# Kernel tuning notes

Hardware: AMD Instinct MI355X
Metric: run time of the kernel (lower is better)

## Reference

```python
import jax, jax.numpy as jnp
import numpy as np

B, N, D, D_MODEL = 4, 2048, 512, 512


def setup_inputs() -> dict:
    key = jax.random.key(0)
    kx, kq, kk, kv, ks = jax.random.split(key, 5)
    scale = 1.0 / np.sqrt(D)
    x = jax.random.normal(kx, (B, N, D), dtype=jnp.float32)
    Wq = (jax.random.normal(kq, (D, D_MODEL), dtype=jnp.float32) * scale)
    Wk = (jax.random.normal(kk, (D, D_MODEL), dtype=jnp.float32) * scale)
    Wv = (jax.random.normal(kv, (D, D_MODEL), dtype=jnp.float32) * scale)
    Ws = (jax.random.normal(ks, (D, 1), dtype=jnp.float32) * scale)
    return {"x": x, "Wq": Wq, "Wk": Wk, "Wv": Wv, "Ws": Ws}


def reference(x, Wq, Wk, Wv, Ws):
    # Projections (Linear, no bias)
    Q = x @ Wq                      # (B, N, d_model)
    K = x @ Wk                      # (B, N, d_model)
    V = x @ Wv                      # (B, N, d_model)
    sigma = x @ Ws                  # (B, N, 1)

    n = x.shape[1]
    dm = Wq.shape[1]

    # Prior association: Gaussian kernel over |i-j| distance, row-normalized
    idx = jnp.arange(n)
    dist = jnp.abs(idx[:, None] - idx[None, :]).astype(x.dtype)      # (N, N)
    inv_norm = 1.0 / (jnp.sqrt(2.0 * jnp.pi).astype(x.dtype) * jnp.abs(sigma))
    gaussian = inv_norm * jnp.exp(-0.5 * jnp.square(dist[None] / sigma))  # (B,N,N)
    P = gaussian / jnp.sum(gaussian, axis=-1, keepdims=True)

    # Series association: scaled dot-product softmax attention
    scores = jnp.einsum('bnd,bmd->bnm', Q, K) / jnp.sqrt(jnp.asarray(dm, x.dtype))
    S = jax.nn.softmax(scores, axis=-1)                               # (B,N,N)

    # Reconstruction
    Z = S @ V                                                          # (B,N,d_model)
    return (Z, P)
```

## Files before the change

kernel.cpp:

```cpp
#include <hip/hip_runtime.h>

typedef float f32x4 __attribute__((ext_vector_type(4)));
typedef short s16x8 __attribute__((ext_vector_type(8)));
typedef unsigned short us4 __attribute__((ext_vector_type(4)));

#define MFMA16(a, b, c) __builtin_amdgcn_mfma_f32_16x16x32_bf16(a, b, c, 0, 0, 0)

#define GLOAD_LDS16(gp, lp) __builtin_amdgcn_global_load_lds( \
    (__attribute__((address_space(1))) void*)(gp),            \
    (__attribute__((address_space(3))) void*)(lp), 16, 0, 0)

__device__ __forceinline__ unsigned short f2bf(float f) {
    union { float f; unsigned u; } v; v.f = f;
    unsigned r = v.u + 0x7fffu + ((v.u >> 16) & 1u);
    return (unsigned short)(r >> 16);
}

__device__ __forceinline__ void gemm_core(
    const unsigned short* __restrict__ Ab, size_t Astride,
    const unsigned short* __restrict__ Bb, size_t Bstride,
    int K, unsigned short* As, unsigned short* Bs,
    int t, f32x4 acc[4][4])
{
    const int wave = t >> 6, lane = t & 63;
    const int c = lane & 15, quad = lane >> 4;
    const int wm = (wave >> 1) * 64, wn = (wave & 1) * 64;
    const int srow = t >> 2;
    const int scol = (t & 3) * 8;

    for (int k0 = 0; k0 < K; k0 += 32) {
        __syncthreads();
        const unsigned short* ga = Ab + (size_t)srow * Astride + k0 + scol;
        const unsigned short* gb = Bb + (size_t)srow * Bstride + k0 + scol;
        GLOAD_LDS16(ga,                 As + t * 8);
        GLOAD_LDS16(ga + 64 * Astride,  As + 2048 + t * 8);
        GLOAD_LDS16(gb,                 Bs + t * 8);
        GLOAD_LDS16(gb + 64 * Bstride,  Bs + 2048 + t * 8);
        __syncthreads();

        s16x8 af[4], bf[4];
        #pragma unroll
        for (int i = 0; i < 4; i++)
            af[i] = *(const s16x8*)(As + (wm + i * 16 + c) * 32 + quad * 8);
        #pragma unroll
        for (int i = 0; i < 4; i++)
            bf[i] = *(const s16x8*)(Bs + (wn + i * 16 + c) * 32 + quad * 8);
        #pragma unroll
        for (int mt = 0; mt < 4; mt++)
            #pragma unroll
            for (int nt = 0; nt < 4; nt++)
                acc[mt][nt] = MFMA16(af[mt], bf[nt], acc[mt][nt]);
    }
}

__global__ __launch_bounds__(256) void k_convert(
    const float* __restrict__ x, const float* __restrict__ wq,
    const float* __restrict__ wk, const float* __restrict__ wv,
    unsigned short* __restrict__ xbf, unsigned short* __restrict__ wt,
    float* __restrict__ lg)
{
    int bid = blockIdx.x, t = threadIdx.x;
    if (bid < 4096) {
        int gid = bid * 256 + t;
        float4 v = ((const float4*)x)[gid];
        us4 o = { f2bf(v.x), f2bf(v.y), f2bf(v.z), f2bf(v.w) };
        ((us4*)xbf)[gid] = o;
    } else if (bid < 7168) {
        int idx = (bid - 4096) * 256 + t;
        int w = idx >> 18;
        int r = idx & 262143;
        int k = r >> 9, n = r & 511;
        const float* src = (w == 0) ? wq : (w == 1) ? wk : wv;
        wt[((size_t)(w * 512 + n) << 9) + k] = f2bf(src[r]);
    } else {
        lg[(bid - 7168) * 256 + t] = 0.f;
    }
}

__global__ __launch_bounds__(256) void k_proj(
    const unsigned short* __restrict__ xbf, const unsigned short* __restrict__ wt,
    unsigned short* __restrict__ qbf, unsigned short* __restrict__ kbf,
    unsigned short* __restrict__ vtbf)
{
    __shared__ __align__(16) unsigned short As[128 * 32];
    __shared__ __align__(16) unsigned short Bs[128 * 32];

    int t = threadIdx.x;
    int m0 = blockIdx.x * 128, n0 = blockIdx.y * 128;
    f32x4 acc[4][4] = {};

    gemm_core(xbf + (size_t)m0 * 512, 512, wt + (size_t)n0 * 512, 512,
              512, As, Bs, t, acc);

    int wave = t >> 6, lane = t & 63, c = lane & 15, quad = lane >> 4;
    int wm = (wave >> 1) * 64, wn = (wave & 1) * 64;
    int sel = blockIdx.y >> 2;

    if (sel < 2) {
        unsigned short* dst = sel ? kbf : qbf;
        int ncol0 = n0 - sel * 512;
        #pragma unroll
        for (int mt = 0; mt < 4; mt++) {
            #pragma unroll
            for (int nt = 0; nt < 4; nt++) {
                int col = ncol0 + wn + nt * 16 + c;
                #pragma unroll
                for (int r = 0; r < 4; r++) {
                    int rw = m0 + wm + mt * 16 + quad * 4 + r;
                    dst[(size_t)rw * 512 + col] = f2bf(acc[mt][nt][r]);
                }
            }
        }
    } else {
        #pragma unroll
        for (int mt = 0; mt < 4; mt++) {
            int rw0 = m0 + wm + mt * 16 + quad * 4;
            int bb = rw0 >> 11, nn = rw0 & 2047;
            #pragma unroll
            for (int nt = 0; nt < 4; nt++) {
                int d = (n0 - 1024) + wn + nt * 16 + c;
                us4 pk = { f2bf(acc[mt][nt][0]), f2bf(acc[mt][nt][1]),
                           f2bf(acc[mt][nt][2]), f2bf(acc[mt][nt][3]) };
                *(us4*)(vtbf + ((size_t)(bb * 512 + d)) * 2048 + nn) = pk;
            }
        }
    }
}

__global__ __launch_bounds__(256) void k_score(
    const unsigned short* __restrict__ qbf, const unsigned short* __restrict__ kbf,
    unsigned short* __restrict__ pbf, float* __restrict__ lg)
{
    __shared__ __align__(16) unsigned short As[128 * 32];
    __shared__ __align__(16) unsigned short Bs[128 * 32];

    int t = threadIdx.x;
    int b = blockIdx.z;
    int m0 = blockIdx.x * 128, n0 = blockIdx.y * 128;
    f32x4 acc[4][4] = {};

    gemm_core(qbf + (size_t)(b * 2048 + m0) * 512, 512,
              kbf + (size_t)(b * 2048 + n0) * 512, 512,
              512, As, Bs, t, acc);

    int wave = t >> 6, lane = t & 63, c = lane & 15, quad = lane >> 4;
    int wm = (wave >> 1) * 64, wn = (wave & 1) * 64;
    const float scale = 0.044194173824159216f;

    #pragma unroll
    for (int mt = 0; mt < 4; mt++) {
        #pragma unroll
        for (int r = 0; r < 4; r++) {
            int row = m0 + wm + mt * 16 + quad * 4 + r;
            float rs = 0.f;
            #pragma unroll
            for (int nt = 0; nt < 4; nt++) {
                float p = __expf(acc[mt][nt][r] * scale);
                rs += p;
                pbf[(size_t)(b * 2048 + row) * 2048 + n0 + wn + nt * 16 + c] = f2bf(p);
            }
            rs += __shfl_xor(rs, 1, 16);
            rs += __shfl_xor(rs, 2, 16);
            rs += __shfl_xor(rs, 4, 16);
            rs += __shfl_xor(rs, 8, 16);
            if (c == 0) atomicAdd(&lg[b * 2048 + row], rs);
        }
    }
}

__global__ __launch_bounds__(256) void k_out(
    const unsigned short* __restrict__ pbf, const unsigned short* __restrict__ vtbf,
    const float* __restrict__ lg, float* __restrict__ zout)
{
    __shared__ __align__(16) unsigned short As[128 * 32];
    __shared__ __align__(16) unsigned short Bs[128 * 32];
    __shared__ float invl[128];

    int t = threadIdx.x;
    int b = blockIdx.z;
    int m0 = blockIdx.x * 128, n0 = blockIdx.y * 128;

    if (t < 128) invl[t] = 1.0f / lg[b * 2048 + m0 + t];

    f32x4 acc[4][4] = {};
    gemm_core(pbf + (size_t)(b * 2048 + m0) * 2048, 2048,
              vtbf + (size_t)(b * 512 + n0) * 2048, 2048,
              2048, As, Bs, t, acc);

    int wave = t >> 6, lane = t & 63, c = lane & 15, quad = lane >> 4;
    int wm = (wave >> 1) * 64, wn = (wave & 1) * 64;

    #pragma unroll
    for (int mt = 0; mt < 4; mt++) {
        #pragma unroll
        for (int nt = 0; nt < 4; nt++) {
            #pragma unroll
            for (int r = 0; r < 4; r++) {
                int row = wm + mt * 16 + quad * 4 + r;
                zout[(size_t)(b * 2048 + m0 + row) * 512 + n0 + wn + nt * 16 + c]
                    = acc[mt][nt][r] * invl[row];
            }
        }
    }
}

__global__ __launch_bounds__(256) void k_prior(
    const float* __restrict__ x, const float* __restrict__ wsv,
    float* __restrict__ pout)
{
    __shared__ float red[4];
    __shared__ float red2[4];

    int blk = blockIdx.x;
    int i = blk & 2047;
    int t = threadIdx.x;
    const float* xr = x + (size_t)blk * 512;

    float part = xr[t] * wsv[t] + xr[t + 256] * wsv[t + 256];
    #pragma unroll
    for (int o = 32; o; o >>= 1) part += __shfl_xor(part, o, 64);
    if ((t & 63) == 0) red[t >> 6] = part;
    __syncthreads();
    float sigma = red[0] + red[1] + red[2] + red[3];

    float inv2 = 0.5f / (sigma * sigma);
    float g[8];
    float sum = 0.f;
    #pragma unroll
    for (int u = 0; u < 8; u++) {
        int j = t + u * 256;
        float d = (float)(j - i);
        g[u] = (j == i) ? 1.0f : __expf(-(d * d) * inv2);
        sum += g[u];
    }
    #pragma unroll
    for (int o = 32; o; o >>= 1) sum += __shfl_xor(sum, o, 64);
    if ((t & 63) == 0) red2[t >> 6] = sum;
    __syncthreads();
    float inv = 1.0f / (red2[0] + red2[1] + red2[2] + red2[3]);

    float* pr = pout + (size_t)blk * 2048;
    #pragma unroll
    for (int u = 0; u < 8; u++) pr[t + u * 256] = g[u] * inv;
}

extern "C" void kernel_launch(void* const* d_in, const int* in_sizes, int n_in,
                              void* d_out, int out_size, void* d_ws, size_t ws_size,
                              hipStream_t stream)
{
    const float* x  = (const float*)d_in[0];
    const float* wq = (const float*)d_in[1];
    const float* wk = (const float*)d_in[2];
    const float* wv = (const float*)d_in[3];
    const float* ws = (const float*)d_in[4];

    float* zout = (float*)d_out;
    float* pout = zout + (size_t)4 * 2048 * 512;

    unsigned short* base = (unsigned short*)pout;
    unsigned short* pbf  = base;
    unsigned short* qbf  = base + (size_t)16777216;
    unsigned short* kbf  = qbf  + (size_t)4194304;
    unsigned short* vtbf = kbf  + (size_t)4194304;
    float*          lg   = (float*)(vtbf + (size_t)4194304);
    unsigned short* xbf  = base;
    unsigned short* wt   = base + (size_t)4194304;

    k_convert<<<dim3(7200), dim3(256), 0, stream>>>(x, wq, wk, wv, xbf, wt, lg);
    k_proj  <<<dim3(64, 12),    dim3(256), 0, stream>>>(xbf, wt, qbf, kbf, vtbf);
    k_score <<<dim3(16, 16, 4), dim3(256), 0, stream>>>(qbf, kbf, pbf, lg);
    k_out   <<<dim3(16, 4, 4),  dim3(256), 0, stream>>>(pbf, vtbf, lg, zout);
    k_prior <<<dim3(8192),      dim3(256), 0, stream>>>(x, ws, pout);
}
```

Measured before the change: 213.6 us.

## Use workspace buffers, fuse prior into score kernel, shrink out-GEMM tile

When the workspace is large enough, the intermediates go into it instead of the P output region. That lets the prior computation run in the same launch as the score GEMM, as extra blocks, rather than in a trailing kernel. The output GEMM now uses 128x64 tiles, doubling the block count from 256 to 512 to raise occupancy. The prior kernel writes contiguous float4 stores per thread. The cost is a larger mixed kernel with uneven block work and more B-tile reloads of P in the out GEMM.

```diff
diff --git a/kernel.cpp b/kernel.cpp
--- a/kernel.cpp
+++ b/kernel.cpp
@@ -16,7 +16,7 @@
     return (unsigned short)(r >> 16);
 }
 
-__device__ __forceinline__ void gemm_core(
+__device__ __forceinline__ void gemm_core128(
     const unsigned short* __restrict__ Ab, size_t Astride,
     const unsigned short* __restrict__ Bb, size_t Bstride,
     int K, unsigned short* As, unsigned short* Bs,
@@ -89,8 +89,8 @@
     int m0 = blockIdx.x * 128, n0 = blockIdx.y * 128;
     f32x4 acc[4][4] = {};
 
-    gemm_core(xbf + (size_t)m0 * 512, 512, wt + (size_t)n0 * 512, 512,
-              512, As, Bs, t, acc);
+    gemm_core128(xbf + (size_t)m0 * 512, 512, wt + (size_t)n0 * 512, 512,
+                 512, As, Bs, t, acc);
 
     int wave = t >> 6, lane = t & 63, c = lane & 15, quad = lane >> 4;
     int wm = (wave >> 1) * 64, wn = (wave & 1) * 64;
@@ -127,21 +127,15 @@
     }
 }
 
-__global__ __launch_bounds__(256) void k_score(
+__device__ __forceinline__ void score_body(
     const unsigned short* __restrict__ qbf, const unsigned short* __restrict__ kbf,
-    unsigned short* __restrict__ pbf, float* __restrict__ lg)
-{
-    __shared__ __align__(16) unsigned short As[128 * 32];
-    __shared__ __align__(16) unsigned short Bs[128 * 32];
-
-    int t = threadIdx.x;
-    int b = blockIdx.z;
-    int m0 = blockIdx.x * 128, n0 = blockIdx.y * 128;
+    unsigned short* __restrict__ pbf, float* __restrict__ lg,
+    int b, int m0, int n0, int t, unsigned short* As, unsigned short* Bs)
+{
     f32x4 acc[4][4] = {};
-
-    gemm_core(qbf + (size_t)(b * 2048 + m0) * 512, 512,
-              kbf + (size_t)(b * 2048 + n0) * 512, 512,
-              512, As, Bs, t, acc);
+    gemm_core128(qbf + (size_t)(b * 2048 + m0) * 512, 512,
+                 kbf + (size_t)(b * 2048 + n0) * 512, 512,
+                 512, As, Bs, t, acc);
 
     int wave = t >> 6, lane = t & 63, c = lane & 15, quad = lane >> 4;
     int wm = (wave >> 1) * 64, wn = (wave & 1) * 64;
@@ -168,32 +162,125 @@
     }
 }
 
+__device__ __forceinline__ void prior_body(
+    const float* __restrict__ x, const float* __restrict__ wsv,
+    float* __restrict__ pout, int blk, int t, float* red, float* red2)
+{
+    int i = blk & 2047;
+    const float* xr = x + (size_t)blk * 512;
+
+    float part = xr[t] * wsv[t] + xr[t + 256] * wsv[t + 256];
+    #pragma unroll
+    for (int o = 32; o; o >>= 1) part += __shfl_xor(part, o, 64);
+    if ((t & 63) == 0) red[t >> 6] = part;
+    __syncthreads();
+    float sigma = red[0] + red[1] + red[2] + red[3];
+
+    float inv2 = 0.5f / (sigma * sigma);
+    float g[8];
+    float sum = 0.f;
+    int j0 = t * 8;
+    #pragma unroll
+    for (int u = 0; u < 8; u++) {
+        int j = j0 + u;
+        float d = (float)(j - i);
+        g[u] = (j == i) ? 1.0f : __expf(-(d * d) * inv2);
+        sum += g[u];
+    }
+    #pragma unroll
+    for (int o = 32; o; o >>= 1) sum += __shfl_xor(sum, o, 64);
+    if ((t & 63) == 0) red2[t >> 6] = sum;
+    __syncthreads();
+    float inv = 1.0f / (red2[0] + red2[1] + red2[2] + red2[3]);
+
+    float* pr = pout + (size_t)blk * 2048 + j0;
+    float4 o0 = { g[0] * inv, g[1] * inv, g[2] * inv, g[3] * inv };
+    float4 o1 = { g[4] * inv, g[5] * inv, g[6] * inv, g[7] * inv };
+    ((float4*)pr)[0] = o0;
+    ((float4*)pr)[1] = o1;
+}
+
+__global__ __launch_bounds__(256) void k_score_prior(
+    const unsigned short* __restrict__ qbf, const unsigned short* __restrict__ kbf,
+    unsigned short* __restrict__ pbf, float* __restrict__ lg,
+    const float* __restrict__ x, const float* __restrict__ wsv,
+    float* __restrict__ pout)
+{
+    __shared__ __align__(16) unsigned short As[128 * 32];
+    __shared__ __align__(16) unsigned short Bs[128 * 32];
+    __shared__ float red[4];
+    __shared__ float red2[4];
+
+    int bid = blockIdx.x, t = threadIdx.x;
+    if (bid < 1024) {
+        int b = bid >> 8, r = bid & 255;
+        score_body(qbf, kbf, pbf, lg, b, (r & 15) * 128, (r >> 4) * 128, t, As, Bs);
+    } else {
+        prior_body(x, wsv, pout, bid - 1024, t, red, red2);
+    }
+}
+
+__global__ __launch_bounds__(256) void k_score(
+    const unsigned short* __restrict__ qbf, const unsigned short* __restrict__ kbf,
+    unsigned short* __restrict__ pbf, float* __restrict__ lg)
+{
+    __shared__ __align__(16) unsigned short As[128 * 32];
+    __shared__ __align__(16) unsigned short Bs[128 * 32];
+    score_body(qbf, kbf, pbf, lg, blockIdx.z,
+               blockIdx.x * 128, blockIdx.y * 128, threadIdx.x, As, Bs);
+}
+
 __global__ __launch_bounds__(256) void k_out(
     const unsigned short* __restrict__ pbf, const unsigned short* __restrict__ vtbf,
     const float* __restrict__ lg, float* __restrict__ zout)
 {
     __shared__ __align__(16) unsigned short As[128 * 32];
-    __shared__ __align__(16) unsigned short Bs[128 * 32];
+    __shared__ __align__(16) unsigned short Bs[64 * 32];
     __shared__ float invl[128];
 
     int t = threadIdx.x;
     int b = blockIdx.z;
-    int m0 = blockIdx.x * 128, n0 = blockIdx.y * 128;
+    int m0 = blockIdx.x * 128, n0 = blockIdx.y * 64;
 
     if (t < 128) invl[t] = 1.0f / lg[b * 2048 + m0 + t];
 
-    f32x4 acc[4][4] = {};
-    gemm_core(pbf + (size_t)(b * 2048 + m0) * 2048, 2048,
-              vtbf + (size_t)(b * 512 + n0) * 2048, 2048,
-              2048, As, Bs, t, acc);
-
-    int wave = t >> 6, lane = t & 63, c = lane & 15, quad = lane >> 4;
-    int wm = (wave >> 1) * 64, wn = (wave & 1) * 64;
+    const unsigned short* Ab = pbf + (size_t)(b * 2048 + m0) * 2048;
+    const unsigned short* Bb = vtbf + (size_t)(b * 512 + n0) * 2048;
+
+    const int wave = t >> 6, lane = t & 63;
+    const int c = lane & 15, quad = lane >> 4;
+    const int wm = (wave >> 1) * 64, wn = (wave & 1) * 32;
+    const int srow = t >> 2;
+    const int scol = (t & 3) * 8;
+
+    f32x4 acc[4][2] = {};
+
+    for (int k0 = 0; k0 < 2048; k0 += 32) {
+        __syncthreads();
+        const unsigned short* ga = Ab + (size_t)srow * 2048 + k0 + scol;
+        GLOAD_LDS16(ga,             As + t * 8);
+        GLOAD_LDS16(ga + 64 * 2048, As + 2048 + t * 8);
+        GLOAD_LDS16(Bb + (size_t)srow * 2048 + k0 + scol, Bs + t * 8);
+        __syncthreads();
+
+        s16x8 af[4], bf[2];
+        #pragma unroll
+        for (int i = 0; i < 4; i++)
+            af[i] = *(const s16x8*)(As + (wm + i * 16 + c) * 32 + quad * 8);
+        #pragma unroll
+        for (int i = 0; i < 2; i++)
+            bf[i] = *(const s16x8*)(Bs + (wn + i * 16 + c) * 32 + quad * 8);
+        #pragma unroll
+        for (int mt = 0; mt < 4; mt++)
+            #pragma unroll
+            for (int nt = 0; nt < 2; nt++)
+                acc[mt][nt] = MFMA16(af[mt], bf[nt], acc[mt][nt]);
+    }
 
     #pragma unroll
     for (int mt = 0; mt < 4; mt++) {
         #pragma unroll
-        for (int nt = 0; nt < 4; nt++) {
+        for (int nt = 0; nt < 2; nt++) {
             #pragma unroll
             for (int r = 0; r < 4; r++) {
                 int row = wm + mt * 16 + quad * 4 + r;
@@ -210,38 +297,7 @@
 {
     __shared__ float red[4];
     __shared__ float red2[4];
-
-    int blk = blockIdx.x;
-    int i = blk & 2047;
-    int t = threadIdx.x;
-    const float* xr = x + (size_t)blk * 512;
-
-    float part = xr[t] * wsv[t] + xr[t + 256] * wsv[t + 256];
-    #pragma unroll
-    for (int o = 32; o; o >>= 1) part += __shfl_xor(part, o, 64);
-    if ((t & 63) == 0) red[t >> 6] = part;
-    __syncthreads();
-    float sigma = red[0] + red[1] + red[2] + red[3];
-
-    float inv2 = 0.5f / (sigma * sigma);
-    float g[8];
-    float sum = 0.f;
-    #pragma unroll
-    for (int u = 0; u < 8; u++) {
-        int j = t + u * 256;
-        float d = (float)(j - i);
-        g[u] = (j == i) ? 1.0f : __expf(-(d * d) * inv2);
-        sum += g[u];
-    }
-    #pragma unroll
-    for (int o = 32; o; o >>= 1) sum += __shfl_xor(sum, o, 64);
-    if ((t & 63) == 0) red2[t >> 6] = sum;
-    __syncthreads();
-    float inv = 1.0f / (red2[0] + red2[1] + red2[2] + red2[3]);
-
-    float* pr = pout + (size_t)blk * 2048;
-    #pragma unroll
-    for (int u = 0; u < 8; u++) pr[t + u * 256] = g[u] * inv;
+    prior_body(x, wsv, pout, blockIdx.x, threadIdx.x, red, red2);
 }
 
 extern "C" void kernel_launch(void* const* d_in, const int* in_sizes, int n_in,
@@ -257,18 +313,37 @@
     float* zout = (float*)d_out;
     float* pout = zout + (size_t)4 * 2048 * 512;
 
-    unsigned short* base = (unsigned short*)pout;
-    unsigned short* pbf  = base;
-    unsigned short* qbf  = base + (size_t)16777216;
-    unsigned short* kbf  = qbf  + (size_t)4194304;
-    unsigned short* vtbf = kbf  + (size_t)4194304;
-    float*          lg   = (float*)(vtbf + (size_t)4194304);
-    unsigned short* xbf  = base;
-    unsigned short* wt   = base + (size_t)4194304;
-
-    k_convert<<<dim3(7200), dim3(256), 0, stream>>>(x, wq, wk, wv, xbf, wt, lg);
-    k_proj  <<<dim3(64, 12),    dim3(256), 0, stream>>>(xbf, wt, qbf, kbf, vtbf);
-    k_score <<<dim3(16, 16, 4), dim3(256), 0, stream>>>(qbf, kbf, pbf, lg);
-    k_out   <<<dim3(16, 4, 4),  dim3(256), 0, stream>>>(pbf, vtbf, lg, zout);
-    k_prior <<<dim3(8192),      dim3(256), 0, stream>>>(x, ws, pout);
-}
+    const size_t need = ((size_t)4194304 + 786432 + 3 * 4194304 + 16777216) * 2
+                        + 8192 * 4;
+
+    if (ws_size >= need) {
+        unsigned short* base = (unsigned short*)d_ws;
+        unsigned short* xbf  = base;
+        unsigned short* wt   = xbf  + (size_t)4194304;
+        unsigned short* qbf  = wt   + (size_t)786432;
+        unsigned short* kbf  = qbf  + (size_t)4194304;
+        unsigned short* vtbf = kbf  + (size_t)4194304;
+        unsigned short* pbf  = vtbf + (size_t)4194304;
+        float*          lg   = (float*)(pbf + (size_t)16777216);
+
+        k_convert<<<dim3(7200), dim3(256), 0, stream>>>(x, wq, wk, wv, xbf, wt, lg);
+        k_proj       <<<dim3(64, 12),   dim3(256), 0, stream>>>(xbf, wt, qbf, kbf, vtbf);
+        k_score_prior<<<dim3(9216),     dim3(256), 0, stream>>>(qbf, kbf, pbf, lg, x, ws, pout);
+        k_out        <<<dim3(16, 8, 4), dim3(256), 0, stream>>>(pbf, vtbf, lg, zout);
+    } else {
+        unsigned short* base = (unsigned short*)pout;
+        unsigned short* pbf  = base;
+        unsigned short* qbf  = base + (size_t)16777216;
+        unsigned short* kbf  = qbf  + (size_t)4194304;
+        unsigned short* vtbf = kbf  + (size_t)4194304;
+        float*          lg   = (float*)(vtbf + (size_t)4194304);
+        unsigned short* xbf  = base;
+        unsigned short* wt   = base + (size_t)4194304;
+
+        k_convert<<<dim3(7200), dim3(256), 0, stream>>>(x, wq, wk, wv, xbf, wt, lg);
+        k_proj  <<<dim3(64, 12),    dim3(256), 0, stream>>>(xbf, wt, qbf, kbf, vtbf);
+        k_score <<<dim3(16, 16, 4), dim3(256), 0, stream>>>(qbf, kbf, pbf, lg);
+        k_out   <<<dim3(16, 8, 4),  dim3(256), 0, stream>>>(pbf, vtbf, lg, zout);
+        k_prior <<<dim3(8192),      dim3(256), 0, stream>>>(x, ws, pout);
+    }
+}
```

Result: faster. 208.1 us (-2.6%).
